# Optimization experiments

Hardware: AMD Instinct MI355X
Metric: run time of the kernel (lower is better)

## Reference

```python
import jax, jax.numpy as jnp
import numpy as np

B, S, D, H = 2, 2048, 1024, 16
DK = D // H  # 64

def setup_inputs() -> dict:
    key = jax.random.key(0)
    ks = jax.random.split(key, 8)
    xavier = np.sqrt(6.0 / (D + D))  # xavier_uniform bound for square Linear
    def lin_w(k):
        return jax.random.uniform(k, (D, D), jnp.float32, -xavier, xavier)
    return {
        'Q': jax.random.normal(ks[0], (B, S, D), jnp.float32),
        'length': jax.random.randint(ks[1], (B,), 1, S + 1, jnp.int32),
        'Wq': lin_w(ks[2]), 'bq': jnp.zeros((D,), jnp.float32),
        'Wk': lin_w(ks[3]), 'bk': jnp.zeros((D,), jnp.float32),
        'Wv': lin_w(ks[4]), 'bv': jnp.zeros((D,), jnp.float32),
    }

def reference(Q, length, Wq, bq, Wk, bk, Wv, bv):
    # project and split heads: [B,S,D] -> [B,H,S,DK]
    def heads(x, W, b):
        y = jnp.einsum('bsd,de->bse', x, W) + b
        return y.reshape(B, S, H, DK).transpose(0, 2, 1, 3)
    q = heads(Q, Wq, bq)
    k = heads(Q, Wk, bk)
    v = heads(Q, Wv, bv)
    scores = jnp.einsum('bhqd,bhkd->bhqk', q, k) / np.sqrt(DK)
    scores = jnp.exp(scores)  # NOTE: raw exp, no max-subtraction (faithful)
    # multiplicative key mask: mask[b,k] = k < length[b], broadcast over q,h
    mask = (jnp.arange(S)[None, :] < length[:, None]).astype(scores.dtype)
    scores = scores * mask[:, None, None, :]
    attn = scores / (jnp.sum(scores, axis=-1, keepdims=True) + 1e-8)
    ctx = jnp.einsum('bhqk,bhkd->bhqd', attn, v)
    return ctx.transpose(0, 2, 1, 3).reshape(B, S, D)
```

## Files before the change

kernel.cpp:

```cpp
#include <hip/hip_runtime.h>
#include <hip/hip_bf16.h>

#define B_  2
#define S_  2048
#define D_  1024
#define H_  16
#define DK_ 64
#define M_  (B_ * S_)

typedef short short8 __attribute__((ext_vector_type(8)));
typedef float float4v __attribute__((ext_vector_type(4)));

#define QSCALE 0.18033688011112042f

static __device__ __forceinline__ ushort f32_to_bf16bits(float f) {
    union { __hip_bfloat16 h; ushort u; } cv;
    cv.h = __float2bfloat16(f);
    return cv.u;
}

static __device__ __forceinline__ void glds16(const ushort* g, ushort* l) {
    __builtin_amdgcn_global_load_lds(
        (const __attribute__((address_space(1))) unsigned int*)g,
        (__attribute__((address_space(3))) unsigned int*)l, 16, 0, 0);
}

__global__ __launch_bounds__(256) void prep(
    const float* __restrict__ X, const float* __restrict__ W0,
    const float* __restrict__ W1, const float* __restrict__ W2,
    ushort* __restrict__ Xb, ushort* __restrict__ Wt)
{
    const int z = blockIdx.z;
    const int t = threadIdx.x;

    if (z >= 3) {
        const int blk = (z - 3) * 256 + blockIdx.y * 16 + blockIdx.x;
        const int i = blk * 2048 + t * 8;
        float4v a = *(const float4v*)(X + i);
        float4v b = *(const float4v*)(X + i + 4);
        short8 o;
        o[0] = (short)f32_to_bf16bits(a[0]); o[1] = (short)f32_to_bf16bits(a[1]);
        o[2] = (short)f32_to_bf16bits(a[2]); o[3] = (short)f32_to_bf16bits(a[3]);
        o[4] = (short)f32_to_bf16bits(b[0]); o[5] = (short)f32_to_bf16bits(b[1]);
        o[6] = (short)f32_to_bf16bits(b[2]); o[7] = (short)f32_to_bf16bits(b[3]);
        *(short8*)(Xb + i) = o;
        return;
    }

    const float* W = (z == 0) ? W0 : ((z == 1) ? W1 : W2);
    ushort* out = Wt + (size_t)z * D_ * D_;

    __shared__ ushort tile[64 * 72];
    int n0 = blockIdx.x * 64, k0 = blockIdx.y * 64;
    int r = t >> 3, g = t & 7;

    #pragma unroll
    for (int p = 0; p < 2; ++p) {
        int rr = r + p * 32;
        const float* src = W + (size_t)(k0 + rr) * D_ + n0 + g * 8;
        float4v a = *(const float4v*)src;
        float4v b = *(const float4v*)(src + 4);
        short8 o;
        o[0] = (short)f32_to_bf16bits(a[0]); o[1] = (short)f32_to_bf16bits(a[1]);
        o[2] = (short)f32_to_bf16bits(a[2]); o[3] = (short)f32_to_bf16bits(a[3]);
        o[4] = (short)f32_to_bf16bits(b[0]); o[5] = (short)f32_to_bf16bits(b[1]);
        o[6] = (short)f32_to_bf16bits(b[2]); o[7] = (short)f32_to_bf16bits(b[3]);
        *(short8*)&tile[rr * 72 + g * 8] = o;
    }
    __syncthreads();
    #pragma unroll
    for (int p = 0; p < 2; ++p) {
        int rr = r + p * 32;
        short8 v;
        #pragma unroll
        for (int i = 0; i < 8; ++i)
            v[i] = (short)tile[(g * 8 + i) * 72 + rr];
        *(short8*)(out + (size_t)(n0 + rr) * D_ + k0 + g * 8) = v;
    }
}

__global__ __launch_bounds__(256, 2) void proj_gemm(
    const ushort* __restrict__ X,
    const ushort* __restrict__ Wt,
    const float* __restrict__ b0, const float* __restrict__ b1,
    const float* __restrict__ b2,
    const int* __restrict__ length,
    ushort* __restrict__ qkv)
{
    const int m0 = blockIdx.x * 64, n0 = blockIdx.y * 128;
    const int bidx = m0 >> 11;
    const int s0 = m0 & (S_ - 1);
    const bool kv = (s0 < length[bidx]);

    __shared__ __align__(16) ushort As[64 * 64];
    __shared__ __align__(16) ushort Bs[3][128 * 64];

    const int t = threadIdx.x;
    const int lane = t & 63, wid = t >> 6;
    const int quad = lane >> 4, l16 = lane & 15;
    const int wr = wid >> 1, wc = wid & 1;

    float4v accq[2][4] = {}, acck[2][4] = {}, accv[2][4] = {};

    for (int kt = 0; kt < 16; ++kt) {
        const int k0 = kt * 64;
        __syncthreads();
        #pragma unroll
        for (int j = 0; j < 2; ++j) {
            const int cid = wid * 128 + j * 64 + lane;
            const int row = cid >> 3;
            const int cl  = (cid & 7) ^ (row & 7);
            glds16(X + (size_t)(m0 + row) * D_ + k0 + cl * 8, &As[cid * 8]);
        }
        #pragma unroll
        for (int j = 0; j < 4; ++j) {
            const int cid = wid * 256 + j * 64 + lane;
            const int row = cid >> 3;
            const int cl  = (cid & 7) ^ (row & 7);
            const size_t off = (size_t)(n0 + row) * D_ + k0 + cl * 8;
            glds16(Wt + off, &Bs[0][cid * 8]);
            if (kv) {
                glds16(Wt + (size_t)D_ * D_ + off,     &Bs[1][cid * 8]);
                glds16(Wt + (size_t)2 * D_ * D_ + off, &Bs[2][cid * 8]);
            }
        }
        __syncthreads();

        #pragma unroll
        for (int ks = 0; ks < 2; ++ks) {
            short8 a[2];
            #pragma unroll
            for (int i = 0; i < 2; ++i) {
                const int r = wr * 32 + i * 16 + l16;
                const int ph = (ks * 4 + quad) ^ (r & 7);
                a[i] = *(short8*)&As[r * 64 + ph * 8];
            }
            short8 bq[4];
            #pragma unroll
            for (int j = 0; j < 4; ++j) {
                const int r = wc * 64 + j * 16 + l16;
                const int ph = (ks * 4 + quad) ^ (r & 7);
                bq[j] = *(short8*)&Bs[0][r * 64 + ph * 8];
            }
            #pragma unroll
            for (int i = 0; i < 2; ++i)
                #pragma unroll
                for (int j = 0; j < 4; ++j)
                    accq[i][j] = __builtin_amdgcn_mfma_f32_16x16x32_bf16(
                        a[i], bq[j], accq[i][j], 0, 0, 0);
            if (kv) {
                short8 bk[4], bv[4];
                #pragma unroll
                for (int j = 0; j < 4; ++j) {
                    const int r = wc * 64 + j * 16 + l16;
                    const int ph = (ks * 4 + quad) ^ (r & 7);
                    bk[j] = *(short8*)&Bs[1][r * 64 + ph * 8];
                    bv[j] = *(short8*)&Bs[2][r * 64 + ph * 8];
                }
                #pragma unroll
                for (int i = 0; i < 2; ++i)
                    #pragma unroll
                    for (int j = 0; j < 4; ++j) {
                        acck[i][j] = __builtin_amdgcn_mfma_f32_16x16x32_bf16(
                            a[i], bk[j], acck[i][j], 0, 0, 0);
                        accv[i][j] = __builtin_amdgcn_mfma_f32_16x16x32_bf16(
                            a[i], bv[j], accv[i][j], 0, 0, 0);
                    }
            }
        }
    }

    #pragma unroll
    for (int j = 0; j < 4; ++j) {
        const int col = n0 + wc * 64 + j * 16 + l16;
        const int h = col >> 6, dk = col & (DK_ - 1);
        const float bvq = b0[col], bvk = b1[col], bvv = b2[col];
        #pragma unroll
        for (int i = 0; i < 2; ++i) {
            #pragma unroll
            for (int rr = 0; rr < 4; ++rr) {
                const int row = m0 + wr * 32 + i * 16 + quad * 4 + rr;
                const int s = row & (S_ - 1);
                const size_t hdr = ((size_t)(bidx * H_ + h) * S_ + s) * DK_ + dk;
                qkv[hdr] = f32_to_bf16bits((accq[i][j][rr] + bvq) * QSCALE);
                if (kv) {
                    qkv[(size_t)M_ * D_ + hdr] =
                        f32_to_bf16bits(acck[i][j][rr] + bvk);
                    qkv[(size_t)2 * M_ * D_ +
                        ((size_t)(bidx * H_ + h) * DK_ + dk) * S_ + s] =
                        f32_to_bf16bits(accv[i][j][rr] + bvv);
                }
            }
        }
    }
}

__global__ __launch_bounds__(256, 3) void attention(
    const ushort* __restrict__ qkv, const int* __restrict__ length,
    float* __restrict__ out)
{
    const int b = blockIdx.z, h = blockIdx.y, q0 = blockIdx.x * 128;
    int len = length[b];
    if (len > S_) len = S_;
    if (len < 1) len = 1;
    const int nkt = (len + 63) >> 6;

    const ushort* qb = qkv + ((size_t)(b * H_ + h) * S_ + q0) * DK_;
    const ushort* kb = qkv + (size_t)M_ * D_ + (size_t)(b * H_ + h) * S_ * DK_;
    const ushort* vb = qkv + (size_t)2 * M_ * D_ + (size_t)(b * H_ + h) * DK_ * S_;

    __shared__ __align__(16) ushort QPs[128 * 64];
    __shared__ __align__(16) ushort Ks[2][64 * 64];
    __shared__ __align__(16) ushort Vs[2][64 * 64];

    const int t = threadIdx.x, lane = t & 63, wid = t >> 6;
    const int quad = lane >> 4, l16 = lane & 15;
    const int e8 = (l16 & 7) << 1;

    #pragma unroll
    for (int j = 0; j < 4; ++j) {
        const int cid = wid * 256 + j * 64 + lane;
        const int row = cid >> 3;
        const int cl  = (cid & 7) ^ (row & 7);
        glds16(qb + (size_t)row * DK_ + cl * 8, &QPs[cid * 8]);
    }
    #pragma unroll
    for (int j = 0; j < 2; ++j) {
        const int cid = wid * 128 + j * 64 + lane;
        const int row = cid >> 3;
        const int cl  = (cid & 7) ^ (row & 7);
        glds16(kb + (size_t)row * DK_ + cl * 8, &Ks[0][cid * 8]);
        glds16(vb + (size_t)row * S_ + cl * 8,  &Vs[0][cid * 8]);
    }
    __syncthreads();

    short8 qfrag[2][2];
    #pragma unroll
    for (int st = 0; st < 2; ++st)
        #pragma unroll
        for (int ks = 0; ks < 2; ++ks) {
            const int qrow = wid * 32 + st * 16 + l16;
            const int ph = (ks * 4 + quad) ^ (qrow & 7);
            qfrag[st][ks] = *(short8*)&QPs[qrow * 64 + ph * 8];
        }

    short8 ones8;
    #pragma unroll
    for (int i = 0; i < 8; ++i) ones8[i] = (short)0x3F80;

    float4v cacc[2][4] = {};
    float4v racc[2] = {};

    for (int kt = 0; kt < nkt; ++kt) {
        const int cur = kt & 1, nxt = cur ^ 1;
        if (kt + 1 < nkt) {
            #pragma unroll
            for (int j = 0; j < 2; ++j) {
                const int cid = wid * 128 + j * 64 + lane;
                const int row = cid >> 3;
                const int cl  = (cid & 7) ^ (row & 7);
                glds16(kb + (size_t)((kt + 1) * 64 + row) * DK_ + cl * 8,
                       &Ks[nxt][cid * 8]);
                glds16(vb + (size_t)row * S_ + (kt + 1) * 64 + cl * 8,
                       &Vs[nxt][cid * 8]);
            }
        }

        float4v sacc[2][4] = {};
        #pragma unroll
        for (int ks = 0; ks < 2; ++ks)
            #pragma unroll
            for (int ct = 0; ct < 4; ++ct) {
                const int krow = ct * 16 + l16;
                const int pha = (ks * 4 + quad) ^ (krow & 7);
                short8 ak = *(short8*)&Ks[cur][krow * 64 + pha * 8];
                #pragma unroll
                for (int st = 0; st < 2; ++st)
                    sacc[st][ct] = __builtin_amdgcn_mfma_f32_16x16x32_bf16(
                        ak, qfrag[st][ks], sacc[st][ct], 0, 0, 0);
            }

        const bool full = ((kt + 1) * 64 <= len);
        #pragma unroll
        for (int st = 0; st < 2; ++st) {
            const int qrow = wid * 32 + st * 16 + l16;
            #pragma unroll
            for (int ct = 0; ct < 4; ++ct) {
                float v0 = __builtin_amdgcn_exp2f(sacc[st][ct][0]);
                float v1 = __builtin_amdgcn_exp2f(sacc[st][ct][1]);
                float v2 = __builtin_amdgcn_exp2f(sacc[st][ct][2]);
                float v3 = __builtin_amdgcn_exp2f(sacc[st][ct][3]);
                if (!full) {
                    const int kb0 = kt * 64 + ct * 16 + quad * 4;
                    v0 = (kb0 + 0 < len) ? v0 : 0.f;
                    v1 = (kb0 + 1 < len) ? v1 : 0.f;
                    v2 = (kb0 + 2 < len) ? v2 : 0.f;
                    v3 = (kb0 + 3 < len) ? v3 : 0.f;
                }
                uint2 w;
                w.x = (__float_as_uint(v0) >> 16) | (__float_as_uint(v1) & 0xFFFF0000u);
                w.y = (__float_as_uint(v2) >> 16) | (__float_as_uint(v3) & 0xFFFF0000u);
                const int c8 = (ct * 4 + quad) ^ e8;
                *(uint2*)&QPs[qrow * 64 + c8 * 4] = w;
            }
        }

        short8 ap[2][2];
        #pragma unroll
        for (int st = 0; st < 2; ++st)
            #pragma unroll
            for (int ks = 0; ks < 2; ++ks) {
                const int qrow = wid * 32 + st * 16 + l16;
                const int pp = ((ks * 4 + quad) * 2) ^ e8;
                ap[st][ks] = *(short8*)&QPs[qrow * 64 + pp * 4];
            }
        #pragma unroll
        for (int ks = 0; ks < 2; ++ks) {
            #pragma unroll
            for (int ct = 0; ct < 4; ++ct) {
                const int vrow = ct * 16 + l16;
                const int phv = (ks * 4 + quad) ^ (vrow & 7);
                short8 vv = *(short8*)&Vs[cur][vrow * 64 + phv * 8];
                #pragma unroll
                for (int st = 0; st < 2; ++st)
                    cacc[st][ct] = __builtin_amdgcn_mfma_f32_16x16x32_bf16(
                        ap[st][ks], vv, cacc[st][ct], 0, 0, 0);
            }
            #pragma unroll
            for (int st = 0; st < 2; ++st)
                racc[st] = __builtin_amdgcn_mfma_f32_16x16x32_bf16(
                    ap[st][ks], ones8, racc[st], 0, 0, 0);
        }
        __syncthreads();
    }

    #pragma unroll
    for (int st = 0; st < 2; ++st)
        #pragma unroll
        for (int rr = 0; rr < 4; ++rr) {
            const float inv = 1.0f / (racc[st][rr] + 1e-8f);
            const int q = q0 + wid * 32 + st * 16 + quad * 4 + rr;
            #pragma unroll
            for (int ct = 0; ct < 4; ++ct) {
                const int d = h * 64 + ct * 16 + l16;
                out[((size_t)b * S_ + q) * D_ + d] = cacc[st][ct][rr] * inv;
            }
        }
}

extern "C" void kernel_launch(void* const* d_in, const int* in_sizes, int n_in,
                              void* d_out, int out_size, void* d_ws, size_t ws_size,
                              hipStream_t stream)
{
    const float* Q   = (const float*)d_in[0];
    const int*   len = (const int*)d_in[1];
    const float* Wq  = (const float*)d_in[2];
    const float* bq  = (const float*)d_in[3];
    const float* Wk  = (const float*)d_in[4];
    const float* bk  = (const float*)d_in[5];
    const float* Wv  = (const float*)d_in[6];
    const float* bv  = (const float*)d_in[7];
    float* out = (float*)d_out;

    ushort* ws  = (ushort*)d_ws;
    ushort* Xb  = ws;
    ushort* Wt  = ws + (size_t)M_ * D_;
    ushort* qkv = Wt + (size_t)3 * D_ * D_;

    dim3 gPr(16, 16, 11);
    prep<<<gPr, 256, 0, stream>>>(Q, Wq, Wk, Wv, Xb, Wt);

    dim3 gP(M_ / 64, D_ / 128);
    proj_gemm<<<gP, 256, 0, stream>>>(Xb, Wt, bq, bk, bv, len, qkv);

    dim3 gA(S_ / 128, H_, B_);
    attention<<<gA, 256, 0, stream>>>(qkv, len, out);
}
```

Measured before the change: 162.0 us.

## Load K/V fragments directly from global memory instead of LDS double buffering

The attention kernel drops the shared-memory staging of Q, K and V, along with its double-buffered async global-to-LDS prefetch and the per-tile block barrier. MFMA operand fragments are now read straight from global memory, relying on L2/L1 caching since the four waves of a block share the same K/V tiles. LDS is kept only for the P tile, which each wave writes and reads for its own rows, so no block-wide sync is needed. The occupancy hint drops from 3 to 2 blocks per CU. The cost is that load latency is no longer hidden by prefetching, and each wave issues redundant global loads for the same K/V data.

After: 212.1 us. 1.31x slower.

```diff
diff --git a/kernel.cpp b/kernel.cpp
--- a/kernel.cpp
+++ b/kernel.cpp
@@ -195,7 +195,7 @@
     }
 }
 
-__global__ __launch_bounds__(256, 3) void attention(
+__global__ __launch_bounds__(256, 2) void attention(
     const ushort* __restrict__ qkv, const int* __restrict__ length,
     float* __restrict__ out)
 {
@@ -209,39 +209,20 @@
     const ushort* kb = qkv + (size_t)M_ * D_ + (size_t)(b * H_ + h) * S_ * DK_;
     const ushort* vb = qkv + (size_t)2 * M_ * D_ + (size_t)(b * H_ + h) * DK_ * S_;
 
-    __shared__ __align__(16) ushort QPs[128 * 64];
-    __shared__ __align__(16) ushort Ks[2][64 * 64];
-    __shared__ __align__(16) ushort Vs[2][64 * 64];
+    __shared__ __align__(16) ushort Ps[128 * 64];
 
     const int t = threadIdx.x, lane = t & 63, wid = t >> 6;
     const int quad = lane >> 4, l16 = lane & 15;
     const int e8 = (l16 & 7) << 1;
 
-    #pragma unroll
-    for (int j = 0; j < 4; ++j) {
-        const int cid = wid * 256 + j * 64 + lane;
-        const int row = cid >> 3;
-        const int cl  = (cid & 7) ^ (row & 7);
-        glds16(qb + (size_t)row * DK_ + cl * 8, &QPs[cid * 8]);
-    }
-    #pragma unroll
-    for (int j = 0; j < 2; ++j) {
-        const int cid = wid * 128 + j * 64 + lane;
-        const int row = cid >> 3;
-        const int cl  = (cid & 7) ^ (row & 7);
-        glds16(kb + (size_t)row * DK_ + cl * 8, &Ks[0][cid * 8]);
-        glds16(vb + (size_t)row * S_ + cl * 8,  &Vs[0][cid * 8]);
-    }
-    __syncthreads();
-
     short8 qfrag[2][2];
     #pragma unroll
     for (int st = 0; st < 2; ++st)
         #pragma unroll
         for (int ks = 0; ks < 2; ++ks) {
-            const int qrow = wid * 32 + st * 16 + l16;
-            const int ph = (ks * 4 + quad) ^ (qrow & 7);
-            qfrag[st][ks] = *(short8*)&QPs[qrow * 64 + ph * 8];
+            const int q = wid * 32 + st * 16 + l16;
+            qfrag[st][ks] =
+                *(const short8*)(qb + (size_t)q * DK_ + (ks * 4 + quad) * 8);
         }
 
     short8 ones8;
@@ -252,33 +233,23 @@
     float4v racc[2] = {};
 
     for (int kt = 0; kt < nkt; ++kt) {
-        const int cur = kt & 1, nxt = cur ^ 1;
-        if (kt + 1 < nkt) {
-            #pragma unroll
-            for (int j = 0; j < 2; ++j) {
-                const int cid = wid * 128 + j * 64 + lane;
-                const int row = cid >> 3;
-                const int cl  = (cid & 7) ^ (row & 7);
-                glds16(kb + (size_t)((kt + 1) * 64 + row) * DK_ + cl * 8,
-                       &Ks[nxt][cid * 8]);
-                glds16(vb + (size_t)row * S_ + (kt + 1) * 64 + cl * 8,
-                       &Vs[nxt][cid * 8]);
-            }
-        }
-
         float4v sacc[2][4] = {};
         #pragma unroll
-        for (int ks = 0; ks < 2; ++ks)
+        for (int ks = 0; ks < 2; ++ks) {
+            short8 kf[4];
             #pragma unroll
             for (int ct = 0; ct < 4; ++ct) {
-                const int krow = ct * 16 + l16;
-                const int pha = (ks * 4 + quad) ^ (krow & 7);
-                short8 ak = *(short8*)&Ks[cur][krow * 64 + pha * 8];
+                const int key = kt * 64 + ct * 16 + l16;
+                kf[ct] = *(const short8*)(kb + (size_t)key * DK_ +
+                                          (ks * 4 + quad) * 8);
+            }
+            #pragma unroll
+            for (int ct = 0; ct < 4; ++ct)
                 #pragma unroll
                 for (int st = 0; st < 2; ++st)
                     sacc[st][ct] = __builtin_amdgcn_mfma_f32_16x16x32_bf16(
-                        ak, qfrag[st][ks], sacc[st][ct], 0, 0, 0);
-            }
+                        kf[ct], qfrag[st][ks], sacc[st][ct], 0, 0, 0);
+        }
 
         const bool full = ((kt + 1) * 64 <= len);
         #pragma unroll
@@ -301,37 +272,34 @@
                 w.x = (__float_as_uint(v0) >> 16) | (__float_as_uint(v1) & 0xFFFF0000u);
                 w.y = (__float_as_uint(v2) >> 16) | (__float_as_uint(v3) & 0xFFFF0000u);
                 const int c8 = (ct * 4 + quad) ^ e8;
-                *(uint2*)&QPs[qrow * 64 + c8 * 4] = w;
-            }
-        }
-
-        short8 ap[2][2];
-        #pragma unroll
-        for (int st = 0; st < 2; ++st)
-            #pragma unroll
-            for (int ks = 0; ks < 2; ++ks) {
+                *(uint2*)&Ps[qrow * 64 + c8 * 4] = w;
+            }
+        }
+
+        #pragma unroll
+        for (int ks = 0; ks < 2; ++ks) {
+            short8 ap[2];
+            #pragma unroll
+            for (int st = 0; st < 2; ++st) {
                 const int qrow = wid * 32 + st * 16 + l16;
                 const int pp = ((ks * 4 + quad) * 2) ^ e8;
-                ap[st][ks] = *(short8*)&QPs[qrow * 64 + pp * 4];
-            }
-        #pragma unroll
-        for (int ks = 0; ks < 2; ++ks) {
+                ap[st] = *(short8*)&Ps[qrow * 64 + pp * 4];
+            }
             #pragma unroll
             for (int ct = 0; ct < 4; ++ct) {
-                const int vrow = ct * 16 + l16;
-                const int phv = (ks * 4 + quad) ^ (vrow & 7);
-                short8 vv = *(short8*)&Vs[cur][vrow * 64 + phv * 8];
+                const int d = ct * 16 + l16;
+                short8 vf = *(const short8*)(vb + (size_t)d * S_ + kt * 64 +
+                                             (ks * 4 + quad) * 8);
                 #pragma unroll
                 for (int st = 0; st < 2; ++st)
                     cacc[st][ct] = __builtin_amdgcn_mfma_f32_16x16x32_bf16(
-                        ap[st][ks], vv, cacc[st][ct], 0, 0, 0);
+                        ap[st], vf, cacc[st][ct], 0, 0, 0);
             }
             #pragma unroll
             for (int st = 0; st < 2; ++st)
                 racc[st] = __builtin_amdgcn_mfma_f32_16x16x32_bf16(
-                    ap[st][ks], ones8, racc[st], 0, 0, 0);
-        }
-        __syncthreads();
+                    ap[st], ones8, racc[st], 0, 0, 0);
+        }
     }
 
     #pragma unroll
```
